# Performance work log

Measured on AMD Instinct MI355X. Metric: run time of the kernel, lower is better.

## Reference

```python
import jax, jax.numpy as jnp
import numpy as np

QB = 127.0  # 2**(8-1) - 1


def ternary_dequant(w):
    # absmean ternary quantization, then dequantize by scale
    scale = jnp.mean(jnp.abs(w))
    w_t = jnp.clip(jnp.round(w / (scale + 1e-8)), -1.0, 1.0)
    w_t = jnp.where(scale == 0.0, jnp.zeros_like(w), w_t)
    return w_t * scale


def activation_quantize(x):
    # per-row (last-dim) absmax int8 fake-quant
    scale = jnp.max(jnp.abs(x), axis=-1, keepdims=True) / QB
    scale = jnp.maximum(scale, 1e-8)
    return jnp.clip(jnp.round(x / scale), -QB, QB) * scale


def setup_inputs() -> dict:
    key = jax.random.key(0)
    kx, kw = jax.random.split(key)
    x = jax.random.normal(kx, (2, 4096, 4096), dtype=jnp.float32)
    # kaiming_uniform-ish init scale; exact init distribution is irrelevant to the math
    bound = 1.0 / np.sqrt(4096)
    weight = jax.random.uniform(kw, (4096, 4096), dtype=jnp.float32,
                                minval=-bound, maxval=bound)
    return {"x": x, "weight": weight}


def reference(x, weight):
    w_q = ternary_dequant(weight)        # [out, in]
    x_q = activation_quantize(x)         # [b, s, in]
    return jnp.einsum('bsi,oi->bso', x_q, w_q)
```

## Files before the change

### kernel.cpp

```cpp
#include <hip/hip_runtime.h>
#include <stdint.h>
#include <stddef.h>


#define K_DIM 4096
#define M_DIM 8192
#define N_DIM 4096

typedef int v4i __attribute__((ext_vector_type(4)));

__device__ __forceinline__ void async_copy16(void* lds, const void* g) {
  __builtin_amdgcn_global_load_lds(
      (const __attribute__((address_space(1))) unsigned int*)g,
      (__attribute__((address_space(3))) unsigned int*)lds,
      16, 0, 0);
}

__global__ void k_wsum(const float* __restrict__ w, double* __restrict__ partials) {
  const float4* w4 = (const float4*)w;
  int tid = blockIdx.x * 256 + threadIdx.x;
  double s = 0.0;
  for (int i = tid; i < 4194304; i += 262144) {
    float4 v = w4[i];
    s += (double)fabsf(v.x) + (double)fabsf(v.y) +
         (double)fabsf(v.z) + (double)fabsf(v.w);
  }
  for (int off = 32; off > 0; off >>= 1) s += __shfl_down(s, off);
  __shared__ double lsum[4];
  int lane = threadIdx.x & 63, wid = threadIdx.x >> 6;
  if (lane == 0) lsum[wid] = s;
  __syncthreads();
  if (threadIdx.x == 0)
    partials[blockIdx.x] = lsum[0] + lsum[1] + lsum[2] + lsum[3];
}

__global__ void k_wscale(const double* __restrict__ partials, float* __restrict__ wscale) {
  double s = 0.0;
  for (int i = threadIdx.x; i < 1024; i += 256) s += partials[i];
  for (int off = 32; off > 0; off >>= 1) s += __shfl_down(s, off);
  __shared__ double lsum[4];
  int lane = threadIdx.x & 63, wid = threadIdx.x >> 6;
  if (lane == 0) lsum[wid] = s;
  __syncthreads();
  if (threadIdx.x == 0) {
    double tot = lsum[0] + lsum[1] + lsum[2] + lsum[3];
    *wscale = (float)(tot / 16777216.0);
  }
}

__global__ void k_wq(const float* __restrict__ w, const float* __restrict__ wscale,
                     char* __restrict__ qw) {
  float d = *wscale + 1e-8f;
  const float4* w4 = (const float4*)w;
  int* q4 = (int*)qw;
  int tid = blockIdx.x * 256 + threadIdx.x;
  for (int i = tid; i < 4194304; i += 524288) {
    float4 v = w4[i];
    int a = (int)fmaxf(fminf(rintf(v.x / d), 1.f), -1.f);
    int b = (int)fmaxf(fminf(rintf(v.y / d), 1.f), -1.f);
    int c = (int)fmaxf(fminf(rintf(v.z / d), 1.f), -1.f);
    int e = (int)fmaxf(fminf(rintf(v.w / d), 1.f), -1.f);
    q4[i] = (a & 255) | ((b & 255) << 8) | ((c & 255) << 16) | ((e & 255) << 24);
  }
}

__global__ void k_xq(const float* __restrict__ x, char* __restrict__ qx,
                     float* __restrict__ sx) {
  int row = blockIdx.x;
  const float4* xr = (const float4*)(x + (size_t)row * K_DIM);
  float4 v[4];
  float m = 0.f;
#pragma unroll
  for (int c = 0; c < 4; c++) {
    v[c] = xr[threadIdx.x + c * 256];
    m = fmaxf(m, fmaxf(fmaxf(fabsf(v[c].x), fabsf(v[c].y)),
                       fmaxf(fabsf(v[c].z), fabsf(v[c].w))));
  }
  for (int off = 32; off > 0; off >>= 1) m = fmaxf(m, __shfl_down(m, off));
  __shared__ float lm[4];
  __shared__ float bscale;
  int lane = threadIdx.x & 63, wid = threadIdx.x >> 6;
  if (lane == 0) lm[wid] = m;
  __syncthreads();
  if (threadIdx.x == 0) {
    float mm = fmaxf(fmaxf(lm[0], lm[1]), fmaxf(lm[2], lm[3]));
    float sc = fmaxf(mm / 127.0f, 1e-8f);
    bscale = sc;
    sx[row] = sc;
  }
  __syncthreads();
  float sc = bscale;
  int* q4 = (int*)(qx + (size_t)row * K_DIM);
#pragma unroll
  for (int c = 0; c < 4; c++) {
    int a = (int)fmaxf(fminf(rintf(v[c].x / sc), 127.f), -127.f);
    int b = (int)fmaxf(fminf(rintf(v[c].y / sc), 127.f), -127.f);
    int cc = (int)fmaxf(fminf(rintf(v[c].z / sc), 127.f), -127.f);
    int e = (int)fmaxf(fminf(rintf(v[c].w / sc), 127.f), -127.f);
    q4[threadIdx.x + c * 256] = (a & 255) | ((b & 255) << 8) | ((cc & 255) << 16) | ((e & 255) << 24);
  }
}

__global__ __launch_bounds__(512, 2) void k_gemm(const char* __restrict__ qx,
                       const char* __restrict__ qw,
                       const float* __restrict__ sx,
                       const float* __restrict__ wscale,
                       float* __restrict__ out) {
  __shared__ char lds[4][32768];

  const int tid = threadIdx.x;
  const int lane = tid & 63;
  const int wave = tid >> 6;
  const int wr = wave >> 2;
  const int wc = wave & 3;

  const int wg = (blockIdx.x & 7) * 64 + (blockIdx.x >> 3);
  const int bm = wg >> 4;
  const int bn = wg & 15;
  const int rowBase = bm * 256;
  const int colBase = bn * 256;

  const int rl = tid >> 2;
  const int kswz = (((tid & 3) ^ ((rl >> 1) & 3)) << 4);
  const char* gA0 = qx + (size_t)(rowBase + rl) * K_DIM + kswz;
  const char* gA1 = gA0 + (size_t)128 * K_DIM;
  const char* gB0 = qw + (size_t)(colBase + rl) * K_DIM + kswz;
  const char* gB1 = gB0 + (size_t)128 * K_DIM;
  const int dOff = wave << 10;

  const int sR = ((lane & 15) >> 1) & 3;
  const int kro = (((lane >> 4) ^ sR) << 4);
  const int aOff = ((wr << 7) + (lane & 15)) * 64 + kro;
  const int bOff = 16384 + ((wc << 6) + (lane & 15)) * 64 + kro;

  v4i acc[8][4] = {};

  auto STAGE = [&](int t) {
    char* b = &lds[t & 3][0];
    const size_t ko = (size_t)t << 6;
    async_copy16(b + dOff,         gA0 + ko);
    async_copy16(b + 8192 + dOff,  gA1 + ko);
    async_copy16(b + 16384 + dOff, gB0 + ko);
    async_copy16(b + 24576 + dOff, gB1 + ko);
  };

  auto COMPUTE = [&](int t) {
    const char* b = &lds[t & 3][0];
    v4i bf[4];
#pragma unroll
    for (int n = 0; n < 4; ++n)
      bf[n] = *(const v4i*)(b + bOff + n * 1024);
    __builtin_amdgcn_s_setprio(1);
#pragma unroll
    for (int m = 0; m < 8; ++m) {
      v4i af = *(const v4i*)(b + aOff + m * 1024);
#pragma unroll
      for (int n = 0; n < 4; ++n)
        acc[m][n] = __builtin_amdgcn_mfma_i32_16x16x64_i8(af, bf[n], acc[m][n], 0, 0, 0);
    }
    __builtin_amdgcn_s_setprio(0);
  };

  STAGE(0); STAGE(1); STAGE(2);

  for (int t = 0; t < 61; ++t) {
    asm volatile("s_waitcnt vmcnt(8)" ::: "memory");
    __builtin_amdgcn_s_barrier();
    STAGE(t + 3);
    COMPUTE(t);
  }
  asm volatile("s_waitcnt vmcnt(8)" ::: "memory");
  __builtin_amdgcn_s_barrier();
  COMPUTE(61);
  asm volatile("s_waitcnt vmcnt(4)" ::: "memory");
  __builtin_amdgcn_s_barrier();
  COMPUTE(62);
  asm volatile("s_waitcnt vmcnt(0)" ::: "memory");
  __builtin_amdgcn_s_barrier();
  COMPUTE(63);

  const float swv = *wscale;
  const int col0 = colBase + (wc << 6) + (lane & 15);
  const int row0 = rowBase + (wr << 7) + ((lane >> 4) << 2);
#pragma unroll
  for (int m = 0; m < 8; ++m) {
#pragma unroll
    for (int r = 0; r < 4; ++r) {
      const int row = row0 + m * 16 + r;
      const float s = sx[row] * swv;
#pragma unroll
      for (int n = 0; n < 4; ++n)
        out[(size_t)row * N_DIM + col0 + n * 16] = (float)acc[m][n][r] * s;
    }
  }
}

extern "C" void kernel_launch(void* const* d_in, const int* in_sizes, int n_in,
                              void* d_out, int out_size, void* d_ws, size_t ws_size,
                              hipStream_t stream) {
  const float* x = (const float*)d_in[0];
  const float* w = (const float*)d_in[1];
  float* out = (float*)d_out;
  char* ws = (char*)d_ws;

  double* partials = (double*)ws;
  float* wscale    = (float*)(ws + 8192);
  float* sx        = (float*)(ws + 8448);
  char*  qw        = ws + 41472;
  char*  qx        = ws + 41472 + 16777216;

  k_wsum  <<<1024, 256, 0, stream>>>(w, partials);
  k_wscale<<<   1, 256, 0, stream>>>(partials, wscale);
  k_wq    <<<2048, 256, 0, stream>>>(w, wscale, qw);
  k_xq    <<<8192, 256, 0, stream>>>(x, qx, sx);
  k_gemm  <<<32 * 16, 512, 0, stream>>>(qx, qw, sx, wscale, out);
}
```

Baseline: 394.6 us.

## Fuse quant kernels, use threshold ternary, switch GEMM to 32x32x32 MFMA

Merges the weight-scale finalize, weight quantization and activation quantization into one launch. Each weight block redundantly reduces the partials and binary-searches a float threshold, so the per-element divide and round becomes two comparisons. The GEMM moves from 16x16x64 to 32x32x32 int8 MFMA with a new LDS fragment mapping and epilogue indexing. Async staging of the next tile is issued after the fragment loads. The fusion cuts launch overhead and the larger MFMA tile reduces LDS reads per MFMA, at the cost of per-block redundant reduction work and threshold-equivalence risk at rounding boundaries.

```diff
diff --git a/kernel.cpp b/kernel.cpp
--- a/kernel.cpp
+++ b/kernel.cpp
@@ -7,7 +7,8 @@
 #define M_DIM 8192
 #define N_DIM 4096
 
-typedef int v4i __attribute__((ext_vector_type(4)));
+typedef int v4i  __attribute__((ext_vector_type(4)));
+typedef int v16i __attribute__((ext_vector_type(16)));
 
 __device__ __forceinline__ void async_copy16(void* lds, const void* g) {
   __builtin_amdgcn_global_load_lds(
@@ -34,70 +35,76 @@
     partials[blockIdx.x] = lsum[0] + lsum[1] + lsum[2] + lsum[3];
 }
 
-__global__ void k_wscale(const double* __restrict__ partials, float* __restrict__ wscale) {
-  double s = 0.0;
-  for (int i = threadIdx.x; i < 1024; i += 256) s += partials[i];
-  for (int off = 32; off > 0; off >>= 1) s += __shfl_down(s, off);
-  __shared__ double lsum[4];
-  int lane = threadIdx.x & 63, wid = threadIdx.x >> 6;
-  if (lane == 0) lsum[wid] = s;
-  __syncthreads();
-  if (threadIdx.x == 0) {
-    double tot = lsum[0] + lsum[1] + lsum[2] + lsum[3];
-    *wscale = (float)(tot / 16777216.0);
-  }
-}
-
-__global__ void k_wq(const float* __restrict__ w, const float* __restrict__ wscale,
-                     char* __restrict__ qw) {
-  float d = *wscale + 1e-8f;
-  const float4* w4 = (const float4*)w;
-  int* q4 = (int*)qw;
-  int tid = blockIdx.x * 256 + threadIdx.x;
-  for (int i = tid; i < 4194304; i += 524288) {
-    float4 v = w4[i];
-    int a = (int)fmaxf(fminf(rintf(v.x / d), 1.f), -1.f);
-    int b = (int)fmaxf(fminf(rintf(v.y / d), 1.f), -1.f);
-    int c = (int)fmaxf(fminf(rintf(v.z / d), 1.f), -1.f);
-    int e = (int)fmaxf(fminf(rintf(v.w / d), 1.f), -1.f);
-    q4[i] = (a & 255) | ((b & 255) << 8) | ((c & 255) << 16) | ((e & 255) << 24);
-  }
-}
-
-__global__ void k_xq(const float* __restrict__ x, char* __restrict__ qx,
-                     float* __restrict__ sx) {
-  int row = blockIdx.x;
-  const float4* xr = (const float4*)(x + (size_t)row * K_DIM);
-  float4 v[4];
-  float m = 0.f;
-#pragma unroll
-  for (int c = 0; c < 4; c++) {
-    v[c] = xr[threadIdx.x + c * 256];
-    m = fmaxf(m, fmaxf(fmaxf(fabsf(v[c].x), fabsf(v[c].y)),
-                       fmaxf(fabsf(v[c].z), fabsf(v[c].w))));
-  }
-  for (int off = 32; off > 0; off >>= 1) m = fmaxf(m, __shfl_down(m, off));
+__global__ void k_quant(const float* __restrict__ w, const double* __restrict__ partials,
+                        float* __restrict__ wscale, char* __restrict__ qw,
+                        const float* __restrict__ x, char* __restrict__ qx,
+                        float* __restrict__ sx) {
+  __shared__ float sT;
   __shared__ float lm[4];
   __shared__ float bscale;
-  int lane = threadIdx.x & 63, wid = threadIdx.x >> 6;
-  if (lane == 0) lm[wid] = m;
-  __syncthreads();
-  if (threadIdx.x == 0) {
-    float mm = fmaxf(fmaxf(lm[0], lm[1]), fmaxf(lm[2], lm[3]));
-    float sc = fmaxf(mm / 127.0f, 1e-8f);
-    bscale = sc;
-    sx[row] = sc;
-  }
-  __syncthreads();
-  float sc = bscale;
-  int* q4 = (int*)(qx + (size_t)row * K_DIM);
-#pragma unroll
-  for (int c = 0; c < 4; c++) {
-    int a = (int)fmaxf(fminf(rintf(v[c].x / sc), 127.f), -127.f);
-    int b = (int)fmaxf(fminf(rintf(v[c].y / sc), 127.f), -127.f);
-    int cc = (int)fmaxf(fminf(rintf(v[c].z / sc), 127.f), -127.f);
-    int e = (int)fmaxf(fminf(rintf(v[c].w / sc), 127.f), -127.f);
-    q4[threadIdx.x + c * 256] = (a & 255) | ((b & 255) << 8) | ((cc & 255) << 16) | ((e & 255) << 24);
+
+  if (blockIdx.x < 2048) {
+    if (threadIdx.x < 64) {
+      double s = 0.0;
+      for (int i = threadIdx.x; i < 1024; i += 64) s += partials[i];
+      for (int off = 32; off > 0; off >>= 1) s += __shfl_down(s, off);
+      if (threadIdx.x == 0) {
+        float sc = (float)(s / 16777216.0);
+        if (blockIdx.x == 0) *wscale = sc;
+        float d = sc + 1e-8f;
+        unsigned lo = 1u, hi = __float_as_uint(d);
+        while (hi - lo > 1u) {
+          unsigned mid = lo + ((hi - lo) >> 1);
+          if (__uint_as_float(mid) / d > 0.5f) hi = mid; else lo = mid;
+        }
+        sT = __uint_as_float(hi);
+      }
+    }
+    __syncthreads();
+    const float T = sT;
+    const float4* w4 = (const float4*)w;
+    int* q4 = (int*)qw;
+    int tid = blockIdx.x * 256 + threadIdx.x;
+    for (int i = tid; i < 4194304; i += 524288) {
+      float4 v = w4[i];
+      int a = (int)(v.x >= T) - (int)(v.x <= -T);
+      int b = (int)(v.y >= T) - (int)(v.y <= -T);
+      int c = (int)(v.z >= T) - (int)(v.z <= -T);
+      int e = (int)(v.w >= T) - (int)(v.w <= -T);
+      q4[i] = (a & 255) | ((b & 255) << 8) | ((c & 255) << 16) | ((e & 255) << 24);
+    }
+  } else {
+    int row = blockIdx.x - 2048;
+    const float4* xr = (const float4*)(x + (size_t)row * K_DIM);
+    float4 v[4];
+    float m = 0.f;
+#pragma unroll
+    for (int c = 0; c < 4; c++) {
+      v[c] = xr[threadIdx.x + c * 256];
+      m = fmaxf(m, fmaxf(fmaxf(fabsf(v[c].x), fabsf(v[c].y)),
+                         fmaxf(fabsf(v[c].z), fabsf(v[c].w))));
+    }
+    for (int off = 32; off > 0; off >>= 1) m = fmaxf(m, __shfl_down(m, off));
+    int lane = threadIdx.x & 63, wid = threadIdx.x >> 6;
+    if (lane == 0) lm[wid] = m;
+    __syncthreads();
+    if (threadIdx.x == 0) {
+      float mm = fmaxf(fmaxf(lm[0], lm[1]), fmaxf(lm[2], lm[3]));
+      float sc = fmaxf(mm / 127.0f, 1e-8f);
+      bscale = sc;
+      sx[row] = sc;
+    }
+    __syncthreads();
+    float sc = bscale;
+    int* q4 = (int*)(qx + (size_t)row * K_DIM);
+#pragma unroll
+    for (int c = 0; c < 4; c++) {
+      int a = (int)fmaxf(fminf(rintf(v[c].x / sc), 127.f), -127.f);
+      int b = (int)fmaxf(fminf(rintf(v[c].y / sc), 127.f), -127.f);
+      int cc = (int)fmaxf(fminf(rintf(v[c].z / sc), 127.f), -127.f);
+      int e = (int)fmaxf(fminf(rintf(v[c].w / sc), 127.f), -127.f);
+      q4[threadIdx.x + c * 256] = (a & 255) | ((b & 255) << 8) | ((cc & 255) << 16) | ((e & 255) << 24);
+    }
   }
 }
 
@@ -128,12 +135,13 @@
   const char* gB1 = gB0 + (size_t)128 * K_DIM;
   const int dOff = wave << 10;
 
-  const int sR = ((lane & 15) >> 1) & 3;
-  const int kro = (((lane >> 4) ^ sR) << 4);
-  const int aOff = ((wr << 7) + (lane & 15)) * 64 + kro;
-  const int bOff = 16384 + ((wc << 6) + (lane & 15)) * 64 + kro;
-
-  v4i acc[8][4] = {};
+  const int hi = lane >> 5;
+  const int selk = (lane >> 1) & 3;
+  const int colk[2] = { ((hi) ^ selk) << 4, ((2 + hi) ^ selk) << 4 };
+  const int aBase = ((wr << 7) + (lane & 31)) * 64;
+  const int bBase = 16384 + ((wc << 6) + (lane & 31)) * 64;
+
+  v16i acc[4][2] = {};
 
   auto STAGE = [&](int t) {
     char* b = &lds[t & 3][0];
@@ -144,20 +152,30 @@
     async_copy16(b + 24576 + dOff, gB1 + ko);
   };
 
-  auto COMPUTE = [&](int t) {
-    const char* b = &lds[t & 3][0];
-    v4i bf[4];
-#pragma unroll
-    for (int n = 0; n < 4; ++n)
-      bf[n] = *(const v4i*)(b + bOff + n * 1024);
+  auto BODY = [&](int t, bool doStage) {
+    const char* b_ = &lds[t & 3][0];
+    v4i bv[2][2], av[4][2];
+#pragma unroll
+    for (int sn = 0; sn < 2; ++sn)
+#pragma unroll
+      for (int kk = 0; kk < 2; ++kk)
+        bv[sn][kk] = *(const v4i*)(b_ + bBase + sn * 2048 + colk[kk]);
+#pragma unroll
+    for (int sub = 0; sub < 4; ++sub)
+#pragma unroll
+      for (int kk = 0; kk < 2; ++kk)
+        av[sub][kk] = *(const v4i*)(b_ + aBase + sub * 2048 + colk[kk]);
+    if (doStage) STAGE(t + 3);
+    asm volatile("" ::: "memory");
     __builtin_amdgcn_s_setprio(1);
 #pragma unroll
-    for (int m = 0; m < 8; ++m) {
-      v4i af = *(const v4i*)(b + aOff + m * 1024);
-#pragma unroll
-      for (int n = 0; n < 4; ++n)
-        acc[m][n] = __builtin_amdgcn_mfma_i32_16x16x64_i8(af, bf[n], acc[m][n], 0, 0, 0);
-    }
+    for (int kk = 0; kk < 2; ++kk)
+#pragma unroll
+      for (int sub = 0; sub < 4; ++sub)
+#pragma unroll
+        for (int sn = 0; sn < 2; ++sn)
+          acc[sub][sn] = __builtin_amdgcn_mfma_i32_32x32x32_i8(
+              av[sub][kk], bv[sn][kk], acc[sub][sn], 0, 0, 0);
     __builtin_amdgcn_s_setprio(0);
   };
 
@@ -166,31 +184,34 @@
   for (int t = 0; t < 61; ++t) {
     asm volatile("s_waitcnt vmcnt(8)" ::: "memory");
     __builtin_amdgcn_s_barrier();
-    STAGE(t + 3);
-    COMPUTE(t);
+    asm volatile("" ::: "memory");
+    BODY(t, true);
   }
   asm volatile("s_waitcnt vmcnt(8)" ::: "memory");
   __builtin_amdgcn_s_barrier();
-  COMPUTE(61);
+  asm volatile("" ::: "memory");
+  BODY(61, false);
   asm volatile("s_waitcnt vmcnt(4)" ::: "memory");
   __builtin_amdgcn_s_barrier();
-  COMPUTE(62);
+  asm volatile("" ::: "memory");
+  BODY(62, false);
   asm volatile("s_waitcnt vmcnt(0)" ::: "memory");
   __builtin_amdgcn_s_barrier();
-  COMPUTE(63);
+  asm volatile("" ::: "memory");
+  BODY(63, false);
 
   const float swv = *wscale;
-  const int col0 = colBase + (wc << 6) + (lane & 15);
-  const int row0 = rowBase + (wr << 7) + ((lane >> 4) << 2);
-#pragma unroll
-  for (int m = 0; m < 8; ++m) {
-#pragma unroll
-    for (int r = 0; r < 4; ++r) {
-      const int row = row0 + m * 16 + r;
+  const int colE = colBase + (wc << 6) + (lane & 31);
+#pragma unroll
+  for (int sub = 0; sub < 4; ++sub) {
+#pragma unroll
+    for (int reg = 0; reg < 16; ++reg) {
+      const int row = rowBase + (wr << 7) + sub * 32 + 4 * hi +
+                      (reg & 3) + 8 * (reg >> 2);
       const float s = sx[row] * swv;
 #pragma unroll
-      for (int n = 0; n < 4; ++n)
-        out[(size_t)row * N_DIM + col0 + n * 16] = (float)acc[m][n][r] * s;
+      for (int sn = 0; sn < 2; ++sn)
+        out[(size_t)row * N_DIM + colE + sn * 32] = (float)acc[sub][sn][reg] * s;
     }
   }
 }
@@ -209,9 +230,7 @@
   char*  qw        = ws + 41472;
   char*  qx        = ws + 41472 + 16777216;
 
-  k_wsum  <<<1024, 256, 0, stream>>>(w, partials);
-  k_wscale<<<   1, 256, 0, stream>>>(partials, wscale);
-  k_wq    <<<2048, 256, 0, stream>>>(w, wscale, qw);
-  k_xq    <<<8192, 256, 0, stream>>>(x, qx, sx);
-  k_gemm  <<<32 * 16, 512, 0, stream>>>(qx, qw, sx, wscale, out);
-}
+  k_wsum <<<1024, 256, 0, stream>>>(w, partials);
+  k_quant<<<2048 + 8192, 256, 0, stream>>>(w, partials, wscale, qw, x, qx, sx);
+  k_gemm <<<32 * 16, 512, 0, stream>>>(qx, qw, sx, wscale, out);
+}
```

Result: slower. 409.7 us (+3.8%).
